# Performance work log

Hardware: AMD Instinct MI355X
Metric: run time of the kernel (lower is better)

## Reference

```python
import jax, jax.numpy as jnp
import numpy as np

# TT-factorized linear: 784 = 7*4*7*4 -> 512 = 4*4*8*4, max_rank=20
# canonical TT ranks: [1, 20, 20, 16, 1] (r3 capped by m4*n4 = 16)
B = 16384
R1, R2, R3 = 20, 20, 16


def setup_inputs() -> dict:
    key = jax.random.key(0)
    k = jax.random.split(key, 6)
    x = jax.random.normal(k[0], (B, 784), jnp.float32)
    # TT cores G_k[r_{k-1}, m_k, n_k, r_k] with boundary ranks squeezed
    core1 = jax.random.normal(k[1], (7, 4, R1), jnp.float32) * 0.3   # [m1,n1,r1]
    core2 = jax.random.normal(k[2], (R1, 4, 4, R2), jnp.float32) * 0.1  # [r1,m2,n2,r2]
    core3 = jax.random.normal(k[3], (R2, 7, 8, R3), jnp.float32) * 0.05  # [r2,m3,n3,r3]
    core4 = jax.random.normal(k[4], (R3, 4, 4), jnp.float32) * 0.1   # [r3,m4,n4]
    bias = jax.random.normal(k[5], (512,), jnp.float32) * 0.01
    return {"x": x, "core1": core1, "core2": core2, "core3": core3,
            "core4": core4, "bias": bias}


def reference(x, core1, core2, core3, core4, bias):
    b = x.shape[0]
    # reshape input into TT mode factorization [B, m1, m2, m3, m4]
    x5 = x.reshape(b, 7, 4, 7, 4)
    # chain of small core contractions (the fusion-opportunity op pattern)
    t = jnp.einsum('bijkl,ipr->bjklpr', x5, core1)   # [B,4,7,4, n1,r1]
    t = jnp.einsum('bjklpr,rjqs->bklpqs', t, core2)  # [B,7,4, n1,n2,r2]
    t = jnp.einsum('bklpqs,sket->blpqet', t, core3)  # [B,4, n1,n2,n3,r3]
    y = jnp.einsum('blpqet,tlf->bpqef', t, core4)    # [B, n1,n2,n3,n4]
    y = y.reshape(b, 512) + bias
    # original forward: relu then softmax over features.
    # NOTE: the source calls self.fc2(y) but discards the result, so it is
    # omitted here (no effect on output).
    return jax.nn.softmax(jax.nn.relu(y), axis=1)
```

## Files before the change

### kernel.cpp

```cpp
#include <hip/hip_runtime.h>


typedef __attribute__((ext_vector_type(8))) short short8;
typedef __attribute__((ext_vector_type(4))) float floatx4;
typedef __attribute__((address_space(1))) const unsigned int gu32;
typedef __attribute__((address_space(3))) unsigned int lu32;

#define XT_OFF 0
#define WP_OFF 27262976

__device__ __forceinline__ unsigned int pack2_bf16(float a, float b) {
    unsigned int ua = __float_as_uint(a);
    unsigned int ub = __float_as_uint(b);
    return ((ub + 0x8000u) & 0xFFFF0000u) | ((ua + 0x8000u) >> 16);
}

__device__ __forceinline__ short f32_to_bf16_rne(float v) {
    unsigned int u = __float_as_uint(v);
    return (short)(((u + 0x7FFFu + ((u >> 16) & 1)) >> 16) & 0xFFFF);
}

__global__ void conv_x(const float* __restrict__ x, short* __restrict__ xt) {
    const int g = blockIdx.x * 256 + threadIdx.x;
    const int c    = g & 255;
    const int mbkt = g >> 8;
    const int kt = mbkt % 13;
    const int mb = mbkt / 13;
    const int ks = c >> 7, mt = (c >> 6) & 1, quad = (c >> 4) & 3, lid = c & 15;
    const int row = mb * 32 + mt * 16 + lid;
    const int k0  = kt * 64 + ks * 32 + quad * 8;
    floatx4 v0 = {0.f, 0.f, 0.f, 0.f}, v1 = {0.f, 0.f, 0.f, 0.f};
    if (k0 < 784) {
        const floatx4* p = (const floatx4*)(x + (size_t)row * 784 + k0);
        v0 = p[0]; v1 = p[1];
    }
    union { short8 s; unsigned int u[4]; } af;
    af.u[0] = pack2_bf16(v0.x, v0.y);
    af.u[1] = pack2_bf16(v0.z, v0.w);
    af.u[2] = pack2_bf16(v1.x, v1.y);
    af.u[3] = pack2_bf16(v1.z, v1.w);
    *(short8*)(xt + (size_t)g * 8) = af.s;
}

__global__ void prep_all(const float* __restrict__ c1, const float* __restrict__ c2,
                         const float* __restrict__ c3, const float* __restrict__ c4,
                         short* __restrict__ wp) {
    const int tid = threadIdx.x;
    const int blk = blockIdx.x;
    if (blk == 224) {
        for (int e = tid; e < 24576; e += 256) {
            int tn = e / 768;
            int r  = e % 768;
            int qq = r >> 7;
            int lid = (r >> 3) & 15;
            int j  = r & 7;
            int tks  = (qq < 2) ? 24 : 25;
            int quad = (qq < 2) ? (2 + qq) : (qq - 2);
            wp[(((tn * 26 + tks) * 64 + quad * 16 + lid) << 3) + j] = 0;
        }
        return;
    }
    __shared__ float t12s[320];
    __shared__ float t123s[7 * 256];
    __shared__ float c4s[256];

    const int ij    = blk >> 3;
    const int strip = blk & 7;
    const int i  = ij >> 2, j2 = ij & 3;
    const int p  = strip >> 1;
    const int qh = strip & 1;

    if (tid < 256) c4s[tid] = c4[tid];
    for (int e = tid; e < 320; e += 256) {
        int s = e % 20, pq = e / 20;
        int pp = pq >> 2, q = pq & 3;
        float acc = 0.f;
        #pragma unroll
        for (int r = 0; r < 20; ++r)
            acc += c1[i * 80 + pp * 20 + r] * c2[r * 320 + j2 * 80 + q * 20 + s];
        t12s[e] = acc;
    }
    __syncthreads();

    for (int e = tid; e < 1792; e += 256) {
        int k3 = e >> 8, li = e & 255;
        int t = li & 15, pql = li >> 4;
        int qloc = pql >> 3, e3 = pql & 7;
        int q = 2 * qh + qloc;
        float acc = 0.f;
        const float* tp = t12s + (p * 4 + q) * 20;
        const float* cp = c3 + k3 * 128 + e3 * 16 + t;
        #pragma unroll
        for (int s = 0; s < 20; ++s) acc += tp[s] * cp[s * 896];
        t123s[e] = acc;
    }
    __syncthreads();

    for (int e = tid; e < 1792; e += 256) {
        int kl = e >> 6, nl = e & 63;
        int k = ij * 28 + kl;
        int n = strip * 64 + nl;
        int k3 = kl >> 2, l = kl & 3;
        int f4 = n & 3, e3 = (n >> 2) & 7;
        int pql = ((n >> 5) & 1) * 8 + e3;
        const float* tp = t123s + k3 * 256 + pql * 16;
        const float* cq = c4s + l * 4 + f4;
        float a = 0.f;
        #pragma unroll
        for (int t = 0; t < 16; ++t) a += tp[t] * cq[t * 16];
        int tks = k >> 5, quad = (k >> 3) & 3, j = k & 7;
        int tn = n >> 4, lid = n & 15;
        wp[(((tn * 26 + tks) * 64 + quad * 16 + lid) << 3) + j] = f32_to_bf16_rne(a);
    }
}

__global__ __launch_bounds__(512, 4) void tt_gemm(const short* __restrict__ xt,
                                                  const short* __restrict__ wp,
                                                  const float* __restrict__ bias,
                                                  float* __restrict__ out) {
    __shared__ __align__(16) short s_a[2][2048];
    __shared__ float part[8][32];

    const int tid  = threadIdx.x;
    const int w    = tid >> 6;
    const int lane = tid & 63;
    const int quad = lane >> 4;
    const int lid  = lane & 15;
    const int mb   = blockIdx.x;
    const int m_base = mb * 32;

    const short* wpw = wp + ((size_t)(w * 4) * 26 * 64 + lane) * 8;

    auto stage = [&](int kt, int buf) {
        if (w < 4) {
            const short* g = xt + (size_t)(mb * 13 + kt) * 2048 + w * 512 + lane * 8;
            __builtin_amdgcn_global_load_lds((gu32*)g, (lu32*)&s_a[buf][w * 512], 16, 0, 0);
        }
    };

    stage(0, 0);
    __syncthreads();

    floatx4 acc[2][4];
    #pragma unroll
    for (int mt = 0; mt < 2; ++mt)
        #pragma unroll
        for (int nt = 0; nt < 4; ++nt)
            acc[mt][nt] = floatx4{0.f, 0.f, 0.f, 0.f};

    #pragma unroll 1
    for (int kt = 0; kt < 13; ++kt) {
        if (kt + 1 < 13) stage(kt + 1, (kt + 1) & 1);

        const short* sab = &s_a[kt & 1][lane * 8];
        #pragma unroll
        for (int ks = 0; ks < 2; ++ks) {
            short8 a0 = *(const short8*)(sab + (ks * 128) * 8);
            short8 a1 = *(const short8*)(sab + (ks * 128 + 64) * 8);
            const int tks = kt * 2 + ks;
            #pragma unroll
            for (int nt = 0; nt < 4; ++nt) {
                short8 bf = *(const short8*)(wpw + (size_t)(nt * 26 + tks) * 64 * 8);
                acc[0][nt] = __builtin_amdgcn_mfma_f32_16x16x32_bf16(a0, bf, acc[0][nt], 0, 0, 0);
                acc[1][nt] = __builtin_amdgcn_mfma_f32_16x16x32_bf16(a1, bf, acc[1][nt], 0, 0, 0);
            }
        }
        __syncthreads();
    }

    float bias_v[4];
    #pragma unroll
    for (int nt = 0; nt < 4; ++nt)
        bias_v[nt] = bias[w * 64 + nt * 16 + lid];

    #pragma unroll
    for (int mt = 0; mt < 2; ++mt) {
        #pragma unroll
        for (int reg = 0; reg < 4; ++reg) {
            float s = 0.f;
            #pragma unroll
            for (int nt = 0; nt < 4; ++nt) {
                float v = acc[mt][nt][reg] + bias_v[nt];
                v = fmaxf(v, 0.f);
                float e = __expf(v);
                acc[mt][nt][reg] = e;
                s += e;
            }
            s += __shfl_xor(s, 1, 64);
            s += __shfl_xor(s, 2, 64);
            s += __shfl_xor(s, 4, 64);
            s += __shfl_xor(s, 8, 64);
            if (lid == 0) part[w][mt * 16 + quad * 4 + reg] = s;
        }
    }
    __syncthreads();

    #pragma unroll
    for (int mt = 0; mt < 2; ++mt) {
        #pragma unroll
        for (int reg = 0; reg < 4; ++reg) {
            const int row = mt * 16 + quad * 4 + reg;
            float tot = 0.f;
            #pragma unroll
            for (int ww = 0; ww < 8; ++ww) tot += part[ww][row];
            const float inv = 1.0f / tot;
            #pragma unroll
            for (int nt = 0; nt < 4; ++nt)
                out[(size_t)(m_base + row) * 512 + w * 64 + nt * 16 + lid] = acc[mt][nt][reg] * inv;
        }
    }
}

extern "C" void kernel_launch(void* const* d_in, const int* in_sizes, int n_in,
                              void* d_out, int out_size, void* d_ws, size_t ws_size,
                              hipStream_t stream) {
    const float* x    = (const float*)d_in[0];
    const float* c1   = (const float*)d_in[1];
    const float* c2   = (const float*)d_in[2];
    const float* c3   = (const float*)d_in[3];
    const float* c4   = (const float*)d_in[4];
    const float* bias = (const float*)d_in[5];
    float* out = (float*)d_out;

    char* ws = (char*)d_ws;
    short* xt  = (short*)(ws + XT_OFF);
    short* wpb = (short*)(ws + WP_OFF);

    conv_x  <<<6656, 256, 0, stream>>>(x, xt);
    prep_all<<<225,  256, 0, stream>>>(c1, c2, c3, c4, wpb);
    tt_gemm <<<512,  512, 0, stream>>>(xt, wpb, bias, out);
}
```

Before: 136.1 us.

## Fuse fp32-to-bf16 conversion of x into GEMM and double rows per block

Removes the separate conv_x kernel and its bf16 workspace round trip. The GEMM now loads fp32 x directly, converts it in registers, and writes it into LDS with register-staged prefetch of the next k-tile. Each block now handles 64 rows instead of 32, so B fragments are reused across 4 M-tiles, at the cost of more accumulator registers and lower occupancy (launch bounds 2).

```diff
diff --git a/kernel.cpp b/kernel.cpp
--- a/kernel.cpp
+++ b/kernel.cpp
@@ -3,11 +3,6 @@
 
 typedef __attribute__((ext_vector_type(8))) short short8;
 typedef __attribute__((ext_vector_type(4))) float floatx4;
-typedef __attribute__((address_space(1))) const unsigned int gu32;
-typedef __attribute__((address_space(3))) unsigned int lu32;
-
-#define XT_OFF 0
-#define WP_OFF 27262976
 
 __device__ __forceinline__ unsigned int pack2_bf16(float a, float b) {
     unsigned int ua = __float_as_uint(a);
@@ -18,28 +13,6 @@
 __device__ __forceinline__ short f32_to_bf16_rne(float v) {
     unsigned int u = __float_as_uint(v);
     return (short)(((u + 0x7FFFu + ((u >> 16) & 1)) >> 16) & 0xFFFF);
-}
-
-__global__ void conv_x(const float* __restrict__ x, short* __restrict__ xt) {
-    const int g = blockIdx.x * 256 + threadIdx.x;
-    const int c    = g & 255;
-    const int mbkt = g >> 8;
-    const int kt = mbkt % 13;
-    const int mb = mbkt / 13;
-    const int ks = c >> 7, mt = (c >> 6) & 1, quad = (c >> 4) & 3, lid = c & 15;
-    const int row = mb * 32 + mt * 16 + lid;
-    const int k0  = kt * 64 + ks * 32 + quad * 8;
-    floatx4 v0 = {0.f, 0.f, 0.f, 0.f}, v1 = {0.f, 0.f, 0.f, 0.f};
-    if (k0 < 784) {
-        const floatx4* p = (const floatx4*)(x + (size_t)row * 784 + k0);
-        v0 = p[0]; v1 = p[1];
-    }
-    union { short8 s; unsigned int u[4]; } af;
-    af.u[0] = pack2_bf16(v0.x, v0.y);
-    af.u[1] = pack2_bf16(v0.z, v0.w);
-    af.u[2] = pack2_bf16(v1.x, v1.y);
-    af.u[3] = pack2_bf16(v1.z, v1.w);
-    *(short8*)(xt + (size_t)g * 8) = af.s;
 }
 
 __global__ void prep_all(const float* __restrict__ c1, const float* __restrict__ c2,
@@ -114,58 +87,85 @@
     }
 }
 
-__global__ __launch_bounds__(512, 4) void tt_gemm(const short* __restrict__ xt,
+__global__ __launch_bounds__(512, 2) void tt_gemm(const float* __restrict__ x,
                                                   const short* __restrict__ wp,
                                                   const float* __restrict__ bias,
                                                   float* __restrict__ out) {
-    __shared__ __align__(16) short s_a[2][2048];
-    __shared__ float part[8][32];
+    __shared__ __align__(16) short s_a[2][512 * 8];
+    __shared__ float part[8][64];
 
     const int tid  = threadIdx.x;
     const int w    = tid >> 6;
     const int lane = tid & 63;
     const int quad = lane >> 4;
     const int lid  = lane & 15;
-    const int mb   = blockIdx.x;
-    const int m_base = mb * 32;
+    const int m_base = blockIdx.x * 64;
+
+    const int srow = tid >> 3;
+    const int sk8  = tid & 7;
+    const int sc   = (sk8 >> 2) * 256 + (srow >> 4) * 64 + (sk8 & 3) * 16 + (srow & 15);
+    const float* xrow = x + (size_t)(m_base + srow) * 784 + sk8 * 8;
+    short* sdst0 = &s_a[0][sc * 8];
+    short* sdst1 = &s_a[1][sc * 8];
 
     const short* wpw = wp + ((size_t)(w * 4) * 26 * 64 + lane) * 8;
 
-    auto stage = [&](int kt, int buf) {
-        if (w < 4) {
-            const short* g = xt + (size_t)(mb * 13 + kt) * 2048 + w * 512 + lane * 8;
-            __builtin_amdgcn_global_load_lds((gu32*)g, (lu32*)&s_a[buf][w * 512], 16, 0, 0);
-        }
-    };
-
-    stage(0, 0);
-    __syncthreads();
-
-    floatx4 acc[2][4];
-    #pragma unroll
-    for (int mt = 0; mt < 2; ++mt)
+    {
+        const floatx4* p = (const floatx4*)xrow;
+        floatx4 v0 = p[0], v1 = p[1];
+        union { short8 s; unsigned int u[4]; } af;
+        af.u[0] = pack2_bf16(v0.x, v0.y);
+        af.u[1] = pack2_bf16(v0.z, v0.w);
+        af.u[2] = pack2_bf16(v1.x, v1.y);
+        af.u[3] = pack2_bf16(v1.z, v1.w);
+        *(short8*)sdst0 = af.s;
+    }
+    __syncthreads();
+
+    floatx4 acc[4][4];
+    #pragma unroll
+    for (int mt = 0; mt < 4; ++mt)
         #pragma unroll
         for (int nt = 0; nt < 4; ++nt)
             acc[mt][nt] = floatx4{0.f, 0.f, 0.f, 0.f};
 
     #pragma unroll 1
     for (int kt = 0; kt < 13; ++kt) {
-        if (kt + 1 < 13) stage(kt + 1, (kt + 1) & 1);
+        floatx4 h0 = {0.f, 0.f, 0.f, 0.f}, h1 = {0.f, 0.f, 0.f, 0.f};
+        if (kt < 12) {
+            const int kg = (kt + 1) * 64 + sk8 * 8;
+            if (kg < 784) {
+                const floatx4* p = (const floatx4*)(xrow + (kt + 1) * 64);
+                h0 = p[0]; h1 = p[1];
+            }
+        }
 
         const short* sab = &s_a[kt & 1][lane * 8];
         #pragma unroll
         for (int ks = 0; ks < 2; ++ks) {
-            short8 a0 = *(const short8*)(sab + (ks * 128) * 8);
-            short8 a1 = *(const short8*)(sab + (ks * 128 + 64) * 8);
-            const int tks = kt * 2 + ks;
-            #pragma unroll
-            for (int nt = 0; nt < 4; ++nt) {
-                short8 bf = *(const short8*)(wpw + (size_t)(nt * 26 + tks) * 64 * 8);
-                acc[0][nt] = __builtin_amdgcn_mfma_f32_16x16x32_bf16(a0, bf, acc[0][nt], 0, 0, 0);
-                acc[1][nt] = __builtin_amdgcn_mfma_f32_16x16x32_bf16(a1, bf, acc[1][nt], 0, 0, 0);
-            }
-        }
-        __syncthreads();
+            short8 af[4], bf[4];
+            #pragma unroll
+            for (int mt = 0; mt < 4; ++mt)
+                af[mt] = *(const short8*)(sab + (ks * 256 + mt * 64) * 8);
+            #pragma unroll
+            for (int nt = 0; nt < 4; ++nt)
+                bf[nt] = *(const short8*)(wpw + (size_t)(nt * 26 + kt * 2 + ks) * 64 * 8);
+            #pragma unroll
+            for (int nt = 0; nt < 4; ++nt)
+                #pragma unroll
+                for (int mt = 0; mt < 4; ++mt)
+                    acc[mt][nt] = __builtin_amdgcn_mfma_f32_16x16x32_bf16(af[mt], bf[nt], acc[mt][nt], 0, 0, 0);
+        }
+
+        if (kt < 12) {
+            union { short8 s; unsigned int u[4]; } af;
+            af.u[0] = pack2_bf16(h0.x, h0.y);
+            af.u[1] = pack2_bf16(h0.z, h0.w);
+            af.u[2] = pack2_bf16(h1.x, h1.y);
+            af.u[3] = pack2_bf16(h1.z, h1.w);
+            *(short8*)((kt & 1) ? sdst0 : sdst1) = af.s;
+            __syncthreads();
+        }
     }
 
     float bias_v[4];
@@ -174,7 +174,7 @@
         bias_v[nt] = bias[w * 64 + nt * 16 + lid];
 
     #pragma unroll
-    for (int mt = 0; mt < 2; ++mt) {
+    for (int mt = 0; mt < 4; ++mt) {
         #pragma unroll
         for (int reg = 0; reg < 4; ++reg) {
             float s = 0.f;
@@ -196,7 +196,7 @@
     __syncthreads();
 
     #pragma unroll
-    for (int mt = 0; mt < 2; ++mt) {
+    for (int mt = 0; mt < 4; ++mt) {
         #pragma unroll
         for (int reg = 0; reg < 4; ++reg) {
             const int row = mt * 16 + quad * 4 + reg;
@@ -221,12 +221,8 @@
     const float* c4   = (const float*)d_in[4];
     const float* bias = (const float*)d_in[5];
     float* out = (float*)d_out;
-
-    char* ws = (char*)d_ws;
-    short* xt  = (short*)(ws + XT_OFF);
-    short* wpb = (short*)(ws + WP_OFF);
-
-    conv_x  <<<6656, 256, 0, stream>>>(x, xt);
-    prep_all<<<225,  256, 0, stream>>>(c1, c2, c3, c4, wpb);
-    tt_gemm <<<512,  512, 0, stream>>>(xt, wpb, bias, out);
-}
+    short* wpb = (short*)d_ws;
+
+    prep_all<<<225, 256, 0, stream>>>(c1, c2, c3, c4, wpb);
+    tt_gemm <<<256, 512, 0, stream>>>(x, wpb, bias, out);
+}
```

Measured after the change: 131.5 us. -3.4%, faster.
